# Kernel optimization log

Hardware: AMD Instinct MI355X
Metric: run time of the kernel (lower is better)

Reference implementation:

```python
import jax, jax.numpy as jnp
import numpy as np

ALPHA, BETA, GAMMA = 0.05, 0.95, 0.95   # list_weight
TANH_ALPHA = 2.0
GDEP = 2


def _gcn_rnn(x, adp, preA, W, b):
    # GCN type 'RNN': adaptive batched adj + predefined adj
    h = x
    outs = [h]
    for _ in range(GDEP):
        h = (ALPHA * x
             + BETA * jnp.einsum('nvc,nvw->nwc', h, adp)
             + GAMMA * jnp.einsum('nvc,vw->nwc', h, preA))
        outs.append(h)
    return jnp.concatenate(outs, -1) @ W + b


def _gcn_hyper(x, A, W, b):
    h = x
    outs = [h]
    for _ in range(GDEP):
        h = ALPHA * x + GAMMA * jnp.einsum('nvc,vw->nwc', h, A)
        outs.append(h)
    return jnp.concatenate(outs, -1) @ W + b


def _gcn_tgn(x, Ab, W, b):
    h = x
    outs = [h]
    for _ in range(GDEP):
        h = ALPHA * x + GAMMA * jnp.einsum('nvc,nvw->nwc', h, Ab)
        outs.append(h)
    return jnp.concatenate(outs, -1) @ W + b


def setup_inputs() -> dict:
    key = jax.random.key(0)
    ks = jax.random.split(key, 28)
    B, T, N, F = 16, 24, 512, 2
    H, E = 64, 16          # hidden_size, node embedding dim (dims_hyper[-1])
    TGN_OUT = 32
    D_ATTN = 4 * F         # TAttn default dim_out = 4 * dim_in
    p = lambda i, shape: jax.random.normal(ks[i], shape, dtype=jnp.float32) * 0.1
    return {
        'sample': jax.random.normal(ks[0], (B, T, N, F), dtype=jnp.float32),
        'predefined_A': jax.random.uniform(ks[1], (N, N), dtype=jnp.float32),
        'w_query': p(2, (F, D_ATTN)), 'w_key': p(3, (F, D_ATTN)),
        'attn_bias': p(4, (D_ATTN,)), 'attn_trans': p(5, (D_ATTN, 1)),
        'W_tgn': p(6, ((GDEP + 1) * F, TGN_OUT)), 'b_tgn': p(7, (TGN_OUT,)),
        'W_agg1': p(8, ((GDEP + 1) * H, E)), 'b_agg1': p(9, (E,)),
        'W_agg2': p(10, ((GDEP + 1) * H, E)), 'b_agg2': p(11, (E,)),
        'W_srcemb': p(12, (F, E)), 'b_srcemb': p(13, (E,)),
        'W_tgtemb': p(14, (F, E)), 'b_tgtemb': p(15, (E,)),
        'W_gz': p(16, ((GDEP + 1) * (F + H), H)), 'b_gz': p(17, (H,)),
        'W_gr': p(18, ((GDEP + 1) * (F + H), H)), 'b_gr': p(19, (H,)),
        'W_gc': p(20, ((GDEP + 1) * (F + H), H)), 'b_gc': p(21, (H,)),
        'W_short': p(22, (TGN_OUT, F)), 'b_short': p(23, (F,)),
        'W_long': p(24, (H, F)), 'b_long': p(25, (F,)),
        'W_mix': p(26, (TGN_OUT + H, F)), 'b_mix': p(27, (F,)),
    }


def reference(sample, predefined_A, w_query, w_key, attn_bias, attn_trans,
              W_tgn, b_tgn, W_agg1, b_agg1, W_agg2, b_agg2,
              W_srcemb, b_srcemb, W_tgtemb, b_tgtemb,
              W_gz, b_gz, W_gr, b_gr, W_gc, b_gc,
              W_short, b_short, W_long, b_long, W_mix, b_mix):
    B, T, N, F = sample.shape
    H = W_long.shape[0]
    A = predefined_A
    eye = jnp.eye(N, dtype=sample.dtype)

    def gru_step(hidden, graph):
        # hidden: [B,N,H], graph: [B,N,F]
        gs = _gcn_hyper(hidden, A, W_agg1, b_agg1)
        gt = _gcn_hyper(hidden, A, W_agg2, b_agg2)
        nv_s = jnp.tanh(TANH_ALPHA * (graph @ W_srcemb + b_srcemb) * gs)
        nv_t = jnp.tanh(TANH_ALPHA * (graph @ W_tgtemb + b_tgtemb) * gt)
        a = (jnp.einsum('bnd,bmd->bnm', nv_s, nv_t)
             - jnp.einsum('bnd,bmd->bnm', nv_t, nv_s))
        adp = jax.nn.relu(jnp.tanh(TANH_ALPHA * a)) + eye
        adp = adp / adp.sum(-1, keepdims=True)           # row-normalized [B,N,N]
        combined = jnp.concatenate([graph, hidden], -1)
        z = jax.nn.sigmoid(_gcn_rnn(combined, adp, A, W_gz, b_gz))
        r = jax.nn.sigmoid(_gcn_rnn(combined, adp, A, W_gr, b_gr))
        c = jnp.tanh(_gcn_rnn(jnp.concatenate([graph, r * hidden], -1), adp, A, W_gc, b_gc))
        return z * hidden + (1.0 - z) * c

    hidden = jnp.zeros((B, N, H), dtype=sample.dtype)
    graphs = jnp.moveaxis(sample[:, 0:T - 4:4], 1, 0)    # [T', B, N, F]
    hidden = jax.lax.scan(lambda h, g: (gru_step(h, g), None), hidden, graphs)[0]

    # temporal additive attention over the last 4 graphs (TAttn)
    src = sample[:, -4:]                                  # [B,4,N,F]
    tar = sample[:, -1]                                   # [B,N,F]
    q = (tar @ w_query)[:, None, :, None, :]              # [B,1,N,1,D]
    k = (src @ w_key)[:, :, None, :, :]                   # [B,4,1,N,D]
    scores = (jnp.tanh(q + k + attn_bias) @ attn_trans)[..., 0]   # [B,4,N,N]
    attn = jax.nn.softmax(scores, axis=-1)

    # single TGN layer: graph conv with (predefined + attention) adjacency
    Ab = A[None] + attn.reshape(-1, N, N)                 # [B*4,N,N]
    out = _gcn_tgn(src.reshape(-1, N, F), Ab, W_tgn, b_tgn)
    out = jax.nn.relu(out.reshape(B, 4, N, -1))
    tar = out.sum(axis=1)                                 # [B,N,TGN_OUT]

    gat_result = tar @ W_short + b_short                  # [B,N,F]
    hidden = gru_step(hidden, gat_result)
    gru_result = hidden @ W_long + b_long
    final_result = jnp.concatenate([tar, hidden], -1) @ W_mix + b_mix
    return gat_result, gru_result, final_result, attn
```

## Files before the change

### kernel.cpp

```cpp
#include <hip/hip_runtime.h>

#define ALPHA_C 0.05f
#define BETA_C  0.95f
#define GAMMA_C 0.95f

constexpr int B = 16, T = 24, N = 512, F = 2, H = 64, E = 16;
constexpr int DA = 8;
constexpr int CC = F + H;
constexpr int TGN_OC = 32;
constexpr int NPART = 4;
constexpr unsigned MEGA_LDS = 50176;
constexpr int NVB = 512;

__device__ __forceinline__ float fast_rcp(float x) { return __builtin_amdgcn_rcpf(x); }
__device__ __forceinline__ float fast_tanh(float x) {
    return 1.0f - 2.0f * fast_rcp(__expf(2.0f * x) + 1.0f);
}
__device__ __forceinline__ float fast_sigmoid(float x) {
    return fast_rcp(1.0f + __expf(-x));
}

__device__ __forceinline__ void gload16(const float* g, float* l)
{
    __builtin_amdgcn_global_load_lds((const __attribute__((address_space(1))) void*)g,
                                     (__attribute__((address_space(3))) void*)l, 16, 0, 0);
}

__device__ __forceinline__ void gridbar(unsigned* bar, unsigned nb)
{
    __syncthreads();
    if (threadIdx.x == 0) {
        __threadfence();
        unsigned g = __hip_atomic_load(&bar[1], __ATOMIC_RELAXED, __HIP_MEMORY_SCOPE_AGENT);
        unsigned arrived = __hip_atomic_fetch_add(&bar[0], 1u, __ATOMIC_ACQ_REL,
                                                  __HIP_MEMORY_SCOPE_AGENT);
        if (arrived == nb - 1u) {
            __hip_atomic_store(&bar[0], 0u, __ATOMIC_RELAXED, __HIP_MEMORY_SCOPE_AGENT);
            __hip_atomic_fetch_add(&bar[1], 1u, __ATOMIC_RELEASE, __HIP_MEMORY_SCOPE_AGENT);
        } else {
            while (__hip_atomic_load(&bar[1], __ATOMIC_ACQUIRE,
                                     __HIP_MEMORY_SCOPE_AGENT) == g)
                __builtin_amdgcn_s_sleep(4);
        }
        __threadfence();
    }
    __syncthreads();
}

__global__ void scaleA_kernel(const float* __restrict__ A, float* __restrict__ K1)
{
    int i = blockIdx.x * 256 + threadIdx.x;
    K1[i] = GAMMA_C * A[i];
}

__global__ __launch_bounds__(256) void k2_kernel(const float* __restrict__ A,
                                                 float* __restrict__ K2)
{
    __shared__ float rows[16][258];
    __shared__ float cols[256][17];
    const int tid = threadIdx.x;
    const int r0 = blockIdx.y * 16, c0 = blockIdx.x * 16;
    const int rr = tid >> 4, cc = tid & 15;
    float acc = 0.f;
    for (int k0 = 0; k0 < N; k0 += 256) {
#pragma unroll
        for (int it = 0; it < 4; ++it) {
            int l = it * 256 + tid;
            int row = l >> 6, k4 = (l & 63) << 2;
            *(float4*)&rows[row][k4] = *(const float4*)(A + (size_t)(r0 + row) * N + k0 + k4);
        }
#pragma unroll
        for (int it = 0; it < 4; ++it) {
            int l = it * 256 + tid;
            int k = l >> 2, c4 = (l & 3) << 2;
            *(float4*)&cols[k][c4] = *(const float4*)(A + (size_t)(k0 + k) * N + c0 + c4);
        }
        __syncthreads();
#pragma unroll 8
        for (int k = 0; k < 256; ++k) acc += rows[rr][k] * cols[k][cc];
        __syncthreads();
    }
    size_t i = (size_t)(r0 + rr) * N + c0 + cc;
    K2[i] = GAMMA_C * ALPHA_C * A[i] + GAMMA_C * GAMMA_C * acc;
}

template<bool INSUM>
__global__ __launch_bounds__(512) void bmm4_kernel(
    float* __restrict__ out, const float* __restrict__ x, const float* __restrict__ in,
    const float* __restrict__ M)
{
    __shared__ float sh_m[128][64];
    __shared__ float sh_h[64][68];
    constexpr int Crow = CC;
    const size_t pstr = (size_t)B * N * Crow;
    const int tid = threadIdx.x;
    const int b = blockIdx.z, w0 = blockIdx.x * 64, vq = blockIdx.y;
    const int cg = tid & 15;
    const int wg = tid >> 4;
    const int wid = tid >> 6;
    const int lane = tid & 63;

    float acc[2][4] = {{0,0,0,0},{0,0,0,0}};
    float ag[2] = {0.f, 0.f};

    const float* Mb = M + (size_t)b * N * N + (size_t)(vq * 128) * N + w0;
    const float* inb = in + (size_t)b * N * Crow;

#pragma unroll
    for (int it = 0; it < 4; ++it) {
        int row = it * 32 + wid * 4 + (lane >> 4);
        gload16(Mb + (size_t)row * N + ((lane & 15) << 2),
                &sh_m[0][0] + (it * 2048 + wid * 256));
    }

    for (int vt = 0; vt < 2; ++vt) {
        const int v0 = vq * 128 + vt * 64;
        {
            const float2* h0 = (const float2*)(inb + (size_t)v0 * Crow);
            for (int l = tid; l < 64 * 33; l += 512) {
                int row = l / 33, k = (l - row * 33) * 2;
                float2 v = h0[l];
                if (INSUM) {
#pragma unroll
                    for (int j = 1; j < NPART; ++j) {
                        float2 w = ((const float2*)(inb + (size_t)j * pstr + (size_t)v0 * Crow))[l];
                        v.x += w.x; v.y += w.y;
                    }
                }
                *(float2*)&sh_h[row][k] = v;
            }
        }
        __syncthreads();
#pragma unroll 8
        for (int j = 0; j < 64; ++j) {
            float2 mv = *(const float2*)&sh_m[vt * 64 + j][wg << 1];
            float4 hv = *(const float4*)&sh_h[j][cg << 2];
            acc[0][0] += mv.x * hv.x; acc[0][1] += mv.x * hv.y;
            acc[0][2] += mv.x * hv.z; acc[0][3] += mv.x * hv.w;
            acc[1][0] += mv.y * hv.x; acc[1][1] += mv.y * hv.y;
            acc[1][2] += mv.y * hv.z; acc[1][3] += mv.y * hv.w;
            if (cg < 2) {
                float gv = sh_h[j][64 + cg];
                ag[0] += mv.x * gv; ag[1] += mv.y * gv;
            }
        }
        if (vt == 0) __syncthreads();
    }
    float* outp = out + (size_t)vq * pstr + (size_t)b * N * Crow;
    const float* xb = x + (size_t)b * N * Crow;
#pragma unroll
    for (int r = 0; r < 2; ++r) {
        const int w = w0 + (wg << 1) + r;
        const size_t base = (size_t)w * Crow + (cg << 2);
        float o0 = acc[r][0], o1 = acc[r][1], o2 = acc[r][2], o3 = acc[r][3];
        if (vq == 0) {
            o0 += ALPHA_C * xb[base];     o1 += ALPHA_C * xb[base + 1];
            o2 += ALPHA_C * xb[base + 2]; o3 += ALPHA_C * xb[base + 3];
        }
        float2 lo = {o0, o1}, hi = {o2, o3};
        *(float2*)(outp + base) = lo;
        *(float2*)(outp + base + 2) = hi;
        if (cg < 2) {
            size_t gb = (size_t)w * Crow + 64 + cg;
            float v = ag[r];
            if (vq == 0) v += ALPHA_C * xb[gb];
            outp[gb] = v;
        }
    }
}

__global__ __launch_bounds__(512) void hyper5_kernel(
    float* __restrict__ P1, float* __restrict__ P2, const float* __restrict__ hidden,
    const float* __restrict__ K1, const float* __restrict__ K2)
{
    __shared__ float sh_m1[64][64];
    __shared__ float sh_m2[64][64];
    __shared__ float sh_h[64][64];
    const size_t pstr = (size_t)B * N * H;
    const int tid = threadIdx.x;
    const int b = blockIdx.z, w0 = blockIdx.x * 64, vq = blockIdx.y;
    const int cg = tid & 15;
    const int wg = tid >> 4;
    const int wid = tid >> 6;
    const int lane = tid & 63;

    float a1[2][4] = {{0,0,0,0},{0,0,0,0}};
    float a2[2][4] = {{0,0,0,0},{0,0,0,0}};
    const float* inb = hidden + (size_t)b * N * H;

    for (int vt = 0; vt < 2; ++vt) {
        const int v0 = vq * 128 + vt * 64;
#pragma unroll
        for (int it = 0; it < 2; ++it) {
            int row = it * 32 + wid * 4 + (lane >> 4);
            int c4 = (lane & 15) << 2;
// ... 177 lines not shown
    const float2* c2 = (const float2*)(base + nn0 * CC);
    const float2* p1b = (const float2*)(P1 + nn0 * CC);
    const float2* p2b = (const float2*)(P2 + nn0 * CC);
    for (int l = tid; l < 16 * 33; l += nthr) {
        int row = l & 15, kp = l >> 4;
        int idx = row * 33 + kp;
        float2 v = c2[idx];
        Xt[2 * kp][row] = v.x; Xt[2 * kp + 1][row] = v.y;
        float2 a = p1b[idx];
#pragma unroll
        for (int j = 1; j < NPART; ++j) {
            float2 w = ((const float2*)(P1 + (size_t)j * psC + nn0 * CC))[idx];
            a.x += w.x; a.y += w.y;
        }
        Xt[66 + 2 * kp][row] = a.x; Xt[66 + 2 * kp + 1][row] = a.y;
        float2 c = p2b[idx];
#pragma unroll
        for (int j = 1; j < NPART; ++j) {
            float2 w = ((const float2*)(P2 + (size_t)j * psC + nn0 * CC))[idx];
            c.x += w.x; c.y += w.y;
        }
        Xt[132 + 2 * kp][row] = c.x; Xt[132 + 2 * kp + 1][row] = c.y;
    }
}

__global__ __launch_bounds__(256) void zr5_kernel(
    const float* __restrict__ comb, const float* __restrict__ P1, const float* __restrict__ P2,
    const float* __restrict__ Wgz, const float* __restrict__ bgz,
    const float* __restrict__ Wgr, const float* __restrict__ bgr,
    const float* __restrict__ hidden,
    float* __restrict__ z, float* __restrict__ comb2)
{
    __shared__ float Xt[198][20];
    __shared__ float Wl[66][128];
    const int tid = threadIdx.x;
    const size_t nn0 = (size_t)blockIdx.x * 16;

    stage_xt(Xt, comb, P1, P2, nn0, tid, 256);

    const int cp = tid & 63;
    const int rg = tid >> 6;
    float2 bias = (cp < 32) ? *(const float2*)&bgz[2 * cp]
                            : *(const float2*)&bgr[2 * cp - 64];
    float acc[4][2];
#pragma unroll
    for (int r = 0; r < 4; ++r) { acc[r][0] = bias.x; acc[r][1] = bias.y; }

    for (int ch = 0; ch < 3; ++ch) {
        const int sk0 = ch * 66;
        for (int l = tid; l < 66 * 32; l += 256) {
            int j = l >> 5, q = l & 31;
            float4 w = (q < 16)
                ? ((const float4*)(Wgz + (size_t)(sk0 + j) * H))[q]
                : ((const float4*)(Wgr + (size_t)(sk0 + j) * H))[q - 16];
            *(float4*)&Wl[j][q << 2] = w;
        }
        __syncthreads();
#pragma unroll 6
        for (int j = 0; j < 66; ++j) {
            float4 xv = *(const float4*)&Xt[sk0 + j][rg << 2];
            float2 wv = *(const float2*)&Wl[j][cp << 1];
            acc[0][0] += xv.x * wv.x; acc[0][1] += xv.x * wv.y;
            acc[1][0] += xv.y * wv.x; acc[1][1] += xv.y * wv.y;
            acc[2][0] += xv.z * wv.x; acc[2][1] += xv.z * wv.y;
            acc[3][0] += xv.w * wv.x; acc[3][1] += xv.w * wv.y;
        }
        __syncthreads();
    }

    if (cp < 32) {
        const int oc = 2 * cp;
#pragma unroll
        for (int r = 0; r < 4; ++r) {
            size_t nn = nn0 + (rg << 2) + r;
            z[nn * H + oc]     = fast_sigmoid(acc[r][0]);
            z[nn * H + oc + 1] = fast_sigmoid(acc[r][1]);
        }
    } else {
        const int oc = 2 * cp - 64;
#pragma unroll
        for (int r = 0; r < 4; ++r) {
            size_t nn = nn0 + (rg << 2) + r;
            float h0 = hidden[nn * H + oc], h1 = hidden[nn * H + oc + 1];
            comb2[nn * CC + F + oc]     = fast_sigmoid(acc[r][0]) * h0;
            comb2[nn * CC + F + oc + 1] = fast_sigmoid(acc[r][1]) * h1;
        }
    }
    if (tid < 32) {
        int row = tid >> 1, f = tid & 1;
        comb2[(nn0 + row) * CC + f] = Xt[f][row];
    }
}

__global__ __launch_bounds__(256) void cup5_kernel(
    const float* __restrict__ comb2, const float* __restrict__ P1, const float* __restrict__ P2,
    const float* __restrict__ Wgc, const float* __restrict__ bgc,
    const float* __restrict__ z, float* __restrict__ hidden)
{
    __shared__ float Xt[198][20];
    __shared__ float Wl[66][64];
    const int tid = threadIdx.x;
    const size_t nn0 = (size_t)blockIdx.x * 16;

    stage_xt(Xt, comb2, P1, P2, nn0, tid, 256);

    const int cp = tid & 31;
    const int rg = tid >> 5;
    float2 bias = *(const float2*)&bgc[2 * cp];
    float acc[2][2];
#pragma unroll
    for (int r = 0; r < 2; ++r) { acc[r][0] = bias.x; acc[r][1] = bias.y; }

    for (int ch = 0; ch < 3; ++ch) {
        const int sk0 = ch * 66;
        for (int l = tid; l < 66 * 16; l += 256) {
            int j = l >> 4, q = l & 15;
            float4 w = ((const float4*)(Wgc + (size_t)(sk0 + j) * H))[q];
            *(float4*)&Wl[j][q << 2] = w;
        }
        __syncthreads();
#pragma unroll 6
        for (int j = 0; j < 66; ++j) {
            float2 xv = *(const float2*)&Xt[sk0 + j][rg << 1];
            float2 wv = *(const float2*)&Wl[j][cp << 1];
            acc[0][0] += xv.x * wv.x; acc[0][1] += xv.x * wv.y;
            acc[1][0] += xv.y * wv.x; acc[1][1] += xv.y * wv.y;
        }
        __syncthreads();
    }

    const int oc = 2 * cp;
#pragma unroll
    for (int r = 0; r < 2; ++r) {
        size_t nn = nn0 + (rg << 1) + r;
        float cv0 = fast_tanh(acc[r][0]);
        float cv1 = fast_tanh(acc[r][1]);
        float zv0 = z[nn * H + oc],     ho0 = hidden[nn * H + oc];
        float zv1 = z[nn * H + oc + 1], ho1 = hidden[nn * H + oc + 1];
        hidden[nn * H + oc]     = zv0 * ho0 + (1.0f - zv0) * cv0;
        hidden[nn * H + oc + 1] = zv1 * ho1 + (1.0f - zv1) * cv1;
    }
}

struct MegaArgs {
    const float* graph; long gstride; long gadv; int nsteps;
    const float *A;
    const float *Wa1, *ba1, *Wa2, *ba2, *Wsrc, *bsrc, *Wtgt, *btgt;
    const float *Wgz, *bgz, *Wgr, *bgr, *Wgc, *bgc;
    const float *K1, *K2;
    float *hidden, *nvs, *nvt, *Mcomb, *comb, *comb2, *z, *P1, *P2;
    unsigned* bar;
};

__device__ void ph_hyper(const MegaArgs& a, char* smem, int vb)
{
    float* sm1 = (float*)smem;
    float* sm2 = sm1 + 4096;
    float* shh = sm2 + 4096;
    const size_t pstr = (size_t)B * N * H;
    const int tid = threadIdx.x;
    const int w0 = (vb & 7) * 64, vq = (vb >> 3) & 3, b = vb >> 5;
    const int cg = tid & 15, wg = tid >> 4, wid = tid >> 6, lane = tid & 63;
    float a1[2][4] = {{0,0,0,0},{0,0,0,0}};
    float a2[2][4] = {{0,0,0,0},{0,0,0,0}};
    const float* inb = a.hidden + (size_t)b * N * H;

    for (int vt = 0; vt < 2; ++vt) {
        const int v0 = vq * 128 + vt * 64;
#pragma unroll
        for (int it = 0; it < 2; ++it) {
            int row = it * 32 + wid * 4 + (lane >> 4);
            int c4 = (lane & 15) << 2;
            int loff = it * 2048 + wid * 256;
            gload16(a.K1 + (size_t)(v0 + row) * N + w0 + c4, sm1 + loff);
            gload16(a.K2 + (size_t)(v0 + row) * N + w0 + c4, sm2 + loff);
            gload16(inb + (size_t)(v0 + row) * H + c4,       shh + loff);
        }
        __syncthreads();
#pragma unroll 8
        for (int j = 0; j < 64; ++j) {
            float2 m1 = *(const float2*)&sm1[j * 64 + (wg << 1)];
            float2 m2 = *(const float2*)&sm2[j * 64 + (wg << 1)];
            float4 hv = *(const float4*)&shh[j * 64 + (cg << 2)];
            a1[0][0] += m1.x * hv.x; a1[0][1] += m1.x * hv.y;
            a1[0][2] += m1.x * hv.z; a1[0][3] += m1.x * hv.w;
            a1[1][0] += m1.y * hv.x; a1[1][1] += m1.y * hv.y;
            a1[1][2] += m1.y * hv.z; a1[1][3] += m1.y * hv.w;
            a2[0][0] += m2.x * hv.x; a2[0][1] += m2.x * hv.y;
            a2[0][2] += m2.x * hv.z; a2[0][3] += m2.x * hv.w;
            a2[1][0] += m2.y * hv.x; a2[1][1] += m2.y * hv.y;
            a2[1][2] += m2.y * hv.z; a2[1][3] += m2.y * hv.w;
        }
        __syncthreads();
    }
    float* o1 = a.P1 + (size_t)vq * pstr + (size_t)b * N * H;
    float* o2 = a.P2 + (size_t)vq * pstr + (size_t)b * N * H;
#pragma unroll
    for (int r = 0; r < 2; ++r) {
        const int w = w0 + (wg << 1) + r;
        const size_t base = (size_t)w * H + (cg << 2);
        float4 v1 = {a1[r][0], a1[r][1], a1[r][2], a1[r][3]};
        float4 v2 = {a2[r][0], a2[r][1], a2[r][2], a2[r][3]};
        if (vq == 0) {
            float4 xv = *(const float4*)(inb + base);
            v1.x += ALPHA_C * xv.x; v1.y += ALPHA_C * xv.y;
            v1.z += ALPHA_C * xv.z; v1.w += ALPHA_C * xv.w;
            v2.x += ALPHA_C * xv.x; v2.y += ALPHA_C * xv.y;
            v2.z += ALPHA_C * xv.z; v2.w += ALPHA_C * xv.w;
        }
        *(float4*)(o1 + base) = v1;
        *(float4*)(o2 + base) = v2;
    }
}

__device__ void ph_gsgt(const MegaArgs& a, char* smem, const float* graph, int vb)
{
    constexpr size_t psH = (size_t)B * N * H;
    float (*sh)[196]  = (float(*)[196])smem;
    float (*W1t)[196] = (float(*)[196])(smem + 16 * 196 * 4);
    float (*W2t)[196] = (float(*)[196])(smem + 32 * 196 * 4);
    const int tid = threadIdx.x;
    const size_t nn0 = (size_t)vb * 16;
    for (int l = tid; l < 768; l += 512) {
        int seg = l >> 8, rr = (l >> 4) & 15, ee = l & 15;
        int f4 = ((int)nn0 + rr) * 16 + ee;
        float4 v;
        if (seg == 0) {
            v = ((const float4*)a.hidden)[f4];
        } else {
            const float* Pp = (seg == 1) ? a.P1 : a.P2;
            v = ((const float4*)Pp)[f4];
#pragma unroll
            for (int j = 1; j < NPART; ++j) {
                float4 w = ((const float4*)(Pp + (size_t)j * psH))[f4];
                v.x += w.x; v.y += w.y; v.z += w.z; v.w += w.w;
            }
        }
        *(float4*)&sh[rr][seg * 64 + (ee << 2)] = v;
    }
    for (int l = tid; l < 768; l += 512) {
        int sk = l >> 2, q = l & 3;
        float4 w1 = ((const float4*)a.Wa1)[l];
        float4 w2 = ((const float4*)a.Wa2)[l];
        W1t[4 * q + 0][sk] = w1.x; W1t[4 * q + 1][sk] = w1.y;
        W1t[4 * q + 2][sk] = w1.z; W1t[4 * q + 3][sk] = w1.w;
        W2t[4 * q + 0][sk] = w2.x; W2t[4 * q + 1][sk] = w2.y;
        W2t[4 * q + 2][sk] = w2.z; W2t[4 * q + 3][sk] = w2.w;
    }
    __syncthreads();
    const int e = tid & 15, row = (tid >> 4) & 15, which = tid >> 8;
    float acc = which ? a.ba2[e] : a.ba1[e];
    const float (*Wt_)[196] = which ? W2t : W1t;
#pragma unroll 8
    for (int sk = 0; sk < 192; sk += 4) {
        float4 xv = *(const float4*)&sh[row][sk];
        float4 wv = *(const float4*)&Wt_[e][sk];
        acc += xv.x * wv.x + xv.y * wv.y + xv.z * wv.z + xv.w * wv.w;
    }
    size_t nn = nn0 + row;
    int b = (int)(nn >> 9), n = (int)(nn & (N - 1));
    const float* gp = graph + (size_t)b * a.gstride + (size_t)n * F;
    float g0 = gp[0], g1 = gp[1];
    if (which == 0) {
        float es = g0 * a.Wsrc[e] + g1 * a.Wsrc[E + e] + a.bsrc[e];
        a.nvs[nn * E + e] = fast_tanh(2.0f * es * acc);
    } else {
        float et = g0 * a.Wtgt[e] + g1 * a.Wtgt[E + e] + a.btgt[e];
        a.nvt[nn * E + e] = fast_tanh(2.0f * et * acc);
    }
}

__device__ void ph_adp(const MegaArgs& a, char* smem, const float* graph, int vb)
{
    float (*red)[4] = (float(*)[4])smem;
    float* tot = (float*)(smem + 128);
    const int m = threadIdx.x;
    const int b = vb >> 5;
    const int ng = vb & 31;
    const float4* sm = (const float4*)(a.nvs + ((size_t)b * N + m) * E);
    const float4* tm = (const float4*)(a.nvt + ((size_t)b * N + m) * E);
    float4 smv[4], tmv[4];
#pragma unroll
    for (int dd = 0; dd < 4; ++dd) { smv[dd] = sm[dd]; tmv[dd] = tm[dd]; }

    for (int c = 0; c < 4; ++c) {
        const int n0 = (ng + 32 * c) * 4;
        const float4* sn = (const float4*)(a.nvs + ((size_t)b * N + n0) * E);
        const float4* tn = (const float4*)(a.nvt + ((size_t)b * N + n0) * E);
        float a1[4] = {0.f,0.f,0.f,0.f}, a2[4] = {0.f,0.f,0.f,0.f};
#pragma unroll
        for (int dd = 0; dd < 4; ++dd) {
#pragma unroll
            for (int r = 0; r < 4; ++r) {
                float4 snv = sn[r * 4 + dd], tnv = tn[r * 4 + dd];
                a1[r] += snv.x * tmv[dd].x + snv.y * tmv[dd].y + snv.z * tmv[dd].z + snv.w * tmv[dd].w;
                a2[r] += tnv.x * smv[dd].x + tnv.y * smv[dd].y + tnv.z * smv[dd].z + tnv.w * smv[dd].w;
            }
        }
        float p[4];
#pragma unroll
        for (int r = 0; r < 4; ++r) {
            float pv = fmaxf(fast_tanh(2.0f * (a1[r] - a2[r])), 0.0f);
            if (m == n0 + r) pv += 1.0f;
            p[r] = pv;
        }
        float sr[4] = {p[0], p[1], p[2], p[3]};
        for (int o = 32; o > 0; o >>= 1) {
#pragma unroll
            for (int r = 0; r < 4; ++r) sr[r] += __shfl_down(sr[r], o);
        }
        int wid = m >> 6, lane = m & 63;
        if (lane == 0) {
#pragma unroll
            for (int r = 0; r < 4; ++r) red[wid][r] = sr[r];
        }
        __syncthreads();
        if (m < 4) {
            float t = 0.f;
            for (int i = 0; i < 8; ++i) t += red[i][m];
            tot[m] = BETA_C * fast_rcp(t);
        }
        __syncthreads();
#pragma unroll
        for (int r = 0; r < 4; ++r)
            a.Mcomb[((size_t)b * N + n0 + r) * N + m] =
                GAMMA_C * a.A[(size_t)(n0 + r) * N + m] + p[r] * tot[r];
        if (m < 4 * CC) {
            int r = m / CC, k = m - r * CC;
            size_t nn = (size_t)b * N + n0 + r;
            float v;
            if (k < F) v = graph[(size_t)b * a.gstride + (size_t)(n0 + r) * F + k];
            else       v = a.hidden[nn * H + (k - F)];
            a.comb[nn * CC + k] = v;
        }
        __syncthreads();
    }
}

template<bool INSUM>
__device__ void ph_bmm(const MegaArgs& a, char* smem,
                       float* out, const float* x, const float* in, int vb)
{
    float* sh_m = (float*)smem;
    float (*sh_h)[68] = (float(*)[68])(smem + 128 * 64 * 4);
    constexpr int Crow = CC;
    const size_t pstr = (size_t)B * N * Crow;
    const int tid = threadIdx.x;
    const int w0 = (vb & 7) * 64, vq = (vb >> 3) & 3, b = vb >> 5;
    const int cg = tid & 15, wg = tid >> 4, wid = tid >> 6, lane = tid & 63;

    float acc[2][4] = {{0,0,0,0},{0,0,0,0}};
    float ag[2] = {0.f, 0.f};

    const float* Mb = a.Mcomb + (size_t)b * N * N + (size_t)(vq * 128) * N + w0;
    const float* inb = in + (size_t)b * N * Crow;

#pragma unroll
    for (int it = 0; it < 4; ++it) {
        int row = it * 32 + wid * 4 + (lane >> 4);
        gload16(Mb + (size_t)row * N + ((lane & 15) << 2),
                sh_m + (it * 2048 + wid * 256));
    }

    for (int vt = 0; vt < 2; ++vt) {
        const int v0 = vq * 128 + vt * 64;
        {
            const float2* h0 = (const float2*)(inb + (size_t)v0 * Crow);
            for (int l = tid; l < 64 * 33; l += 512) {
                int row = l / 33, k = (l - row * 33) * 2;
                float2 v = h0[l];
                if (INSUM) {
#pragma unroll
                    for (int j = 1; j < NPART; ++j) {
                        float2 w = ((const float2*)(inb + (size_t)j * pstr + (size_t)v0 * Crow))[l];
                        v.x += w.x; v.y += w.y;
                    }
                }
                *(float2*)&sh_h[row][k] = v;
            }
        }
        __syncthreads();
#pragma unroll 8
        for (int j = 0; j < 64; ++j) {
            float2 mv = *(const float2*)&sh_m[(vt * 64 + j) * 64 + (wg << 1)];
            float4 hv = *(const float4*)&sh_h[j][cg << 2];
            acc[0][0] += mv.x * hv.x; acc[0][1] += mv.x * hv.y;
            acc[0][2] += mv.x * hv.z; acc[0][3] += mv.x * hv.w;
            acc[1][0] += mv.y * hv.x; acc[1][1] += mv.y * hv.y;
            acc[1][2] += mv.y * hv.z; acc[1][3] += mv.y * hv.w;
            if (cg < 2) {
                float gv = sh_h[j][64 + cg];
                ag[0] += mv.x * gv; ag[1] += mv.y * gv;
            }
        }
        if (vt == 0) __syncthreads();
    }
    float* outp = out + (size_t)vq * pstr + (size_t)b * N * Crow;
    const float* xb = x + (size_t)b * N * Crow;
#pragma unroll
    for (int r = 0; r < 2; ++r) {
        const int w = w0 + (wg << 1) + r;
        const size_t base = (size_t)w * Crow + (cg << 2);
        float o0 = acc[r][0], o1 = acc[r][1], o2 = acc[r][2], o3 = acc[r][3];
        if (vq == 0) {
            o0 += ALPHA_C * xb[base];     o1 += ALPHA_C * xb[base + 1];
            o2 += ALPHA_C * xb[base + 2]; o3 += ALPHA_C * xb[base + 3];
        }
        float2 lo = {o0, o1}, hi = {o2, o3};
        *(float2*)(outp + base) = lo;
        *(float2*)(outp + base + 2) = hi;
        if (cg < 2) {
            size_t gb = (size_t)w * Crow + 64 + cg;
            float v = ag[r];
            if (vq == 0) v += ALPHA_C * xb[gb];
            outp[gb] = v;
        }
    }
}

__device__ void ph_zr(const MegaArgs& a, char* smem, int vb)
{
    float (*Xt)[20] = (float(*)[20])smem;
    float (*Wl)[128] = (float(*)[128])(smem + 198 * 20 * 4);
    const int tid = threadIdx.x;
    const size_t nn0 = (size_t)vb * 16;

    stage_xt(Xt, a.comb, a.P1, a.P2, nn0, tid, 512);

    const int cp = tid & 63;
    const int rg = tid >> 6;
    float2 bias = (cp < 32) ? *(const float2*)&a.bgz[2 * cp]
                            : *(const float2*)&a.bgr[2 * cp - 64];
    float acc[2][2] = {{bias.x, bias.y}, {bias.x, bias.y}};

    for (int ch = 0; ch < 3; ++ch) {
        const int sk0 = ch * 66;
        for (int l = tid; l < 66 * 32; l += 512) {
            int j = l >> 5, q = l & 31;
            float4 w = (q < 16)
                ? ((const float4*)(a.Wgz + (size_t)(sk0 + j) * H))[q]
                : ((const float4*)(a.Wgr + (size_t)(sk0 + j) * H))[q - 16];
            *(float4*)&Wl[j][q << 2] = w;
        }
        __syncthreads();
#pragma unroll 6
        for (int j = 0; j < 66; ++j) {
            float2 xv = *(const float2*)&Xt[sk0 + j][rg << 1];
            float2 wv = *(const float2*)&Wl[j][cp << 1];
            acc[0][0] += xv.x * wv.x; acc[0][1] += xv.x * wv.y;
            acc[1][0] += xv.y * wv.x; acc[1][1] += xv.y * wv.y;
        }
        __syncthreads();
    }

    if (cp < 32) {
        const int oc = 2 * cp;
#pragma unroll
        for (int r = 0; r < 2; ++r) {
            size_t nn = nn0 + (rg << 1) + r;
            a.z[nn * H + oc]     = fast_sigmoid(acc[r][0]);
            a.z[nn * H + oc + 1] = fast_sigmoid(acc[r][1]);
        }
    } else {
        const int oc = 2 * cp - 64;
#pragma unroll
        for (int r = 0; r < 2; ++r) {
            size_t nn = nn0 + (rg << 1) + r;
            float h0 = a.hidden[nn * H + oc], h1 = a.hidden[nn * H + oc + 1];
            a.comb2[nn * CC + F + oc]     = fast_sigmoid(acc[r][0]) * h0;
            a.comb2[nn * CC + F + oc + 1] = fast_sigmoid(acc[r][1]) * h1;
        }
    }
    if (tid < 32) {
        int row = tid >> 1, f = tid & 1;
        a.comb2[(nn0 + row) * CC + f] = Xt[f][row];
    }
}

__device__ void ph_cup(const MegaArgs& a, char* smem, int vb)
{
    float (*Xt)[20] = (float(*)[20])smem;
    float (*Wl)[64] = (float(*)[64])(smem + 198 * 20 * 4);
    const int tid = threadIdx.x;
    const size_t nn0 = (size_t)vb * 16;

    stage_xt(Xt, a.comb2, a.P1, a.P2, nn0, tid, 512);

    const int cp = tid & 31;
    const int rg = tid >> 5;
    float2 bias = *(const float2*)&a.bgc[2 * cp];
    float acc0 = bias.x, acc1 = bias.y;

    for (int ch = 0; ch < 3; ++ch) {
        const int sk0 = ch * 66;
        for (int l = tid; l < 66 * 16; l += 512) {
            int j = l >> 4, q = l & 15;
            float4 w = ((const float4*)(a.Wgc + (size_t)(sk0 + j) * H))[q];
            *(float4*)&Wl[j][q << 2] = w;
        }
        __syncthreads();
#pragma unroll 6
        for (int j = 0; j < 66; ++j) {
            float xv = Xt[sk0 + j][rg];
            float2 wv = *(const float2*)&Wl[j][cp << 1];
            acc0 += xv * wv.x; acc1 += xv * wv.y;
        }
        __syncthreads();
    }

    const int oc = 2 * cp;
    size_t nn = nn0 + rg;
    float cv0 = fast_tanh(acc0);
    float cv1 = fast_tanh(acc1);
    float zv0 = a.z[nn * H + oc],     ho0 = a.hidden[nn * H + oc];
    float zv1 = a.z[nn * H + oc + 1], ho1 = a.hidden[nn * H + oc + 1];
    a.hidden[nn * H + oc]     = zv0 * ho0 + (1.0f - zv0) * cv0;
    a.hidden[nn * H + oc + 1] = zv1 * ho1 + (1.0f - zv1) * cv1;
}

#define VB_LOOP(body) for (int vb = blockIdx.x; vb < NVB; vb += nbk) { body; __syncthreads(); }

__global__ __launch_bounds__(512, 2) void gru_mega(MegaArgs a)
{
    extern __shared__ float smem_f[];
    char* smem = (char*)smem_f;
    const int nbk = gridDim.x;
    unsigned* bar = a.bar;
    const float* graph = a.graph;
    for (int s = 0; s < a.nsteps; ++s) {
        VB_LOOP(ph_hyper(a, smem, vb));                              gridbar(bar, nbk);
        VB_LOOP(ph_gsgt(a, smem, graph, vb));                        gridbar(bar, nbk);
        VB_LOOP(ph_adp(a, smem, graph, vb));                         gridbar(bar, nbk);
        VB_LOOP(ph_bmm<false>(a, smem, a.P1, a.comb, a.comb, vb));   gridbar(bar, nbk);
        VB_LOOP(ph_bmm<true>(a, smem, a.P2, a.comb, a.P1, vb));      gridbar(bar, nbk);
        VB_LOOP(ph_zr(a, smem, vb));                                 gridbar(bar, nbk);
        VB_LOOP(ph_bmm<false>(a, smem, a.P1, a.comb2, a.comb2, vb)); gridbar(bar, nbk);
        VB_LOOP(ph_bmm<true>(a, smem, a.P2, a.comb2, a.P1, vb));     gridbar(bar, nbk);
        VB_LOOP(ph_cup(a, smem, vb));                                gridbar(bar, nbk);
        graph += a.gadv;
    }
}

__global__ void qk_kernel(const float* __restrict__ sample,
                          const float* __restrict__ wq, const float* __restrict__ wk,
                          const float* __restrict__ attn_bias,
                          float* __restrict__ q, float* __restrict__ kk)
{
    int idx = blockIdx.x * 256 + threadIdx.x;
    if (idx < B * N * DA) {
        int d = idx & 7;
        int n = (idx >> 3) & (N - 1);
        int b = idx >> 12;
        const float* tar = sample + (((size_t)b * T + (T - 1)) * N + n) * F;
        q[idx] = tar[0] * wq[d] + tar[1] * wq[DA + d] + attn_bias[d];
    } else {
        int j = idx - B * N * DA;
        int d = j & 7;
        int n = (j >> 3) & (N - 1);
        int t = (j >> 12) & 3;
        int b = j >> 14;
        const float* s = sample + (((size_t)b * T + (T - 4 + t)) * N + n) * F;
        kk[j] = s[0] * wk[d] + s[1] * wk[DA + d];
    }
}

__global__ __launch_bounds__(256) void scores3_kernel(
    const float* __restrict__ q, const float* __restrict__ kk,
    const float* __restrict__ trans, float* __restrict__ attn)
{
    int bt = blockIdx.y;
    int b = bt >> 2;
    int rbase = blockIdx.x * 16;
    int wid = threadIdx.x >> 6, lane = threadIdx.x & 63;
    const float* kkbt = kk + (size_t)bt * N * DA;
    float* attnbt = attn + (size_t)bt * N * N;
    float tr[8];
#pragma unroll
    for (int d = 0; d < 8; ++d) tr[d] = trans[d];
    for (int i = 0; i < 4; ++i) {
        int n = rbase + wid * 4 + i;
        const float* qp = q + ((size_t)b * N + n) * DA;
        float4 qa = *(const float4*)qp, qb = *(const float4*)(qp + 4);
        float ev[8]; float ssum = 0.f;
#pragma unroll
        for (int k = 0; k < 8; ++k) {
            const float* kp = kkbt + (size_t)(k * 64 + lane) * DA;
            float4 ka = *(const float4*)kp, kb = *(const float4*)(kp + 4);
            float s = fast_tanh(qa.x + ka.x) * tr[0] + fast_tanh(qa.y + ka.y) * tr[1]
                    + fast_tanh(qa.z + ka.z) * tr[2] + fast_tanh(qa.w + ka.w) * tr[3]
                    + fast_tanh(qb.x + kb.x) * tr[4] + fast_tanh(qb.y + kb.y) * tr[5]
                    + fast_tanh(qb.z + kb.z) * tr[6] + fast_tanh(qb.w + kb.w) * tr[7];
            ev[k] = __expf(s);
            ssum += ev[k];
        }
        for (int o = 32; o > 0; o >>= 1) ssum += __shfl_down(ssum, o);
        ssum = __shfl(ssum, 0);
        float rinv = fast_rcp(ssum);
#pragma unroll
        for (int k = 0; k < 8; ++k)
            attnbt[(size_t)n * N + k * 64 + lane] = ev[k] * rinv;
    }
}

__global__ __launch_bounds__(256) void tgn2_kernel(
    const float* __restrict__ A, const float* __restrict__ attn,
    const float* __restrict__ hbase, long hsB, long hsT,
    const float* __restrict__ xbase, long xsB, long xsT,
    float* __restrict__ out)
{
    __shared__ float sh_m[64][65];
    __shared__ float sh_h[64][2];
    int bt = blockIdx.y;
    int w0 = blockIdx.x * 64;
    int tid = threadIdx.x;
    int wl = tid >> 2, c = tid & 1, vh = (tid >> 1) & 1;
    const float* hp = hbase + (size_t)(bt >> 2) * hsB + (size_t)(bt & 3) * hsT;
    const float* ap = attn + (size_t)bt * N * N;
    float acc = 0.f;
    for (int vt = 0; vt < 8; ++vt) {
        int v0 = vt * 64;
#pragma unroll
        for (int it = 0; it < 16; ++it) {
            int l = it * 256 + tid;
            int vr = l >> 6, wc = l & 63;
            size_t gi = (size_t)(v0 + vr) * N + (w0 + wc);
            sh_m[wc][vr] = A[gi] + ap[gi];
        }
        if (tid < 128) sh_h[tid >> 1][tid & 1] = hp[(size_t)(v0 + (tid >> 1)) * F + (tid & 1)];
        __syncthreads();
#pragma unroll
        for (int jj = 0; jj < 32; ++jj) {
            int j = vh * 32 + jj;
            acc += sh_m[wl][j] * sh_h[j][c];
        }
        __syncthreads();
    }
    acc += __shfl_xor(acc, 2);
    if (vh == 0) {
        const float* xp = xbase + (size_t)(bt >> 2) * xsB + (size_t)(bt & 3) * xsT;
        out[((size_t)bt * N + w0 + wl) * F + c] =
            ALPHA_C * xp[(size_t)(w0 + wl) * F + c] + GAMMA_C * acc;
    }
}

__global__ __launch_bounds__(256) void tgn_out_gat_kernel(
    const float* __restrict__ sample,
    const float* __restrict__ th1, const float* __restrict__ th2,
    const float* __restrict__ Wt, const float* __restrict__ bt_,
    const float* __restrict__ Ws, const float* __restrict__ bs,
    float* __restrict__ tar32, float* __restrict__ out0)
{
    __shared__ float sh_t[8][33];
    const int tid = threadIdx.x;
    const int oc = tid & 31;
    const int r = tid >> 5;
    const size_t nn = (size_t)blockIdx.x * 8 + r;
    const int n = (int)(nn & (N - 1));
    const int b = (int)(nn >> 9);
    float acc = 0.f;
    for (int t = 0; t < 4; ++t) {
        int bt = b * 4 + t;
        const float* s = sample + (((size_t)b * T + (T - 4 + t)) * N + n) * F;
        size_t rr = ((size_t)bt * N + n) * F;
        float v = bt_[oc];
        v += s[0] * Wt[0 * TGN_OC + oc] + s[1] * Wt[1 * TGN_OC + oc];
        v += th1[rr] * Wt[2 * TGN_OC + oc] + th1[rr + 1] * Wt[3 * TGN_OC + oc];
        v += th2[rr] * Wt[4 * TGN_OC + oc] + th2[rr + 1] * Wt[5 * TGN_OC + oc];
        acc += fmaxf(v, 0.0f);
    }
    tar32[nn * TGN_OC + oc] = acc;
    sh_t[r][oc] = acc;
    __syncthreads();
    if (tid < 16) {
        int row = tid >> 1, f = tid & 1;
        size_t nn2 = (size_t)blockIdx.x * 8 + row;
        float g = bs[f];
#pragma unroll
        for (int k = 0; k < TGN_OC; ++k) g += sh_t[row][k] * Ws[(size_t)k * F + f];
        out0[nn2 * F + f] = g;
    }
}

__global__ void final_kernel(const float* __restrict__ hidden, const float* __restrict__ tar32,
                             const float* __restrict__ Wl, const float* __restrict__ bl,
                             const float* __restrict__ Wm, const float* __restrict__ bm,
                             float* __restrict__ dout_gru, float* __restrict__ dout_fin)
{
    int idx = blockIdx.x * 256 + threadIdx.x;
    int f = idx & 1;
    int nn = idx >> 1;
    const float* hp = hidden + (size_t)nn * H;
    const float* tp = tar32 + (size_t)nn * TGN_OC;
    float g = bl[f], fin = bm[f];
    for (int k = 0; k < H; ++k) g += hp[k] * Wl[(size_t)k * F + f];
    for (int k = 0; k < TGN_OC; ++k) fin += tp[k] * Wm[(size_t)k * F + f];
    for (int k = 0; k < H; ++k) fin += hp[k] * Wm[(size_t)(TGN_OC + k) * F + f];
    dout_gru[idx] = g;
    dout_fin[idx] = fin;
}

namespace {
struct Ptrs {
    const float *sample, *A, *wq, *wk, *attn_bias, *attn_trans, *Wt, *bt_;
    const float *Wa1, *ba1, *Wa2, *ba2, *Wsrc, *bsrc, *Wtgt, *btgt;
    const float *Wgz, *bgz, *Wgr, *bgr, *Wgc, *bgc, *Wsh, *bsh, *Wl, *bl, *Wm, *bm;
    float *hidden, *nvs, *nvt, *Mcomb, *K1, *K2, *comb, *comb2, *z, *P1, *P2;
    float *q, *kk, *th1, *th2, *tar32;
    unsigned* bar;
};

void gru_step(hipStream_t stream, const Ptrs& p, const float* graph, long gstride)
{
    dim3 bg(8, NPART, B);
    hyper5_kernel<<<bg, 512, 0, stream>>>(p.P1, p.P2, p.hidden, p.K1, p.K2);
    gsgt5_kernel<<<B * N / 16, 256, 0, stream>>>(
        p.hidden, p.P1, p.P2, p.Wa1, p.ba1, p.Wa2, p.ba2, graph, gstride,
        p.Wsrc, p.bsrc, p.Wtgt, p.btgt, p.nvs, p.nvt);
    adp3_kernel<<<dim3(N / 4, B), 512, 0, stream>>>(
        p.nvs, p.nvt, p.A, p.hidden, graph, gstride, p.Mcomb, p.comb);
    bmm4_kernel<false><<<bg, 512, 0, stream>>>(p.P1, p.comb, p.comb, p.Mcomb);
    bmm4_kernel<true><<<bg, 512, 0, stream>>>(p.P2, p.comb, p.P1, p.Mcomb);
    zr5_kernel<<<B * N / 16, 256, 0, stream>>>(
        p.comb, p.P1, p.P2, p.Wgz, p.bgz, p.Wgr, p.bgr, p.hidden, p.z, p.comb2);
    bmm4_kernel<false><<<bg, 512, 0, stream>>>(p.P1, p.comb2, p.comb2, p.Mcomb);
    bmm4_kernel<true><<<bg, 512, 0, stream>>>(p.P2, p.comb2, p.P1, p.Mcomb);
    cup5_kernel<<<B * N / 16, 256, 0, stream>>>(
        p.comb2, p.P1, p.P2, p.Wgc, p.bgc, p.z, p.hidden);
}
}

extern "C" void kernel_launch(void* const* d_in, const int* in_sizes, int n_in,
                              void* d_out, int out_size, void* d_ws, size_t ws_size,
                              hipStream_t stream)
{
    (void)in_sizes; (void)n_in; (void)out_size; (void)ws_size;
    Ptrs p;
    p.sample = (const float*)d_in[0];
    p.A      = (const float*)d_in[1];
    p.wq     = (const float*)d_in[2];
    p.wk     = (const float*)d_in[3];
    p.attn_bias  = (const float*)d_in[4];
    p.attn_trans = (const float*)d_in[5];
    p.Wt  = (const float*)d_in[6];
    p.bt_ = (const float*)d_in[7];
    p.Wa1 = (const float*)d_in[8];
    p.ba1 = (const float*)d_in[9];
    p.Wa2 = (const float*)d_in[10];
    p.ba2 = (const float*)d_in[11];
    p.Wsrc = (const float*)d_in[12];
    p.bsrc = (const float*)d_in[13];
    p.Wtgt = (const float*)d_in[14];
    p.btgt = (const float*)d_in[15];
    p.Wgz = (const float*)d_in[16];
    p.bgz = (const float*)d_in[17];
    p.Wgr = (const float*)d_in[18];
    p.bgr = (const float*)d_in[19];
    p.Wgc = (const float*)d_in[20];
    p.bgc = (const float*)d_in[21];
    p.Wsh = (const float*)d_in[22];
    p.bsh = (const float*)d_in[23];
    p.Wl  = (const float*)d_in[24];
    p.bl  = (const float*)d_in[25];
    p.Wm  = (const float*)d_in[26];
    p.bm  = (const float*)d_in[27];

    float* ws = (float*)d_ws;
    size_t off = 0;
    auto alloc = [&](size_t nelem) { float* r = ws + off; off += nelem; return r; };
    p.hidden = alloc((size_t)B * N * H);
    p.nvs    = alloc((size_t)B * N * E);
    p.nvt    = alloc((size_t)B * N * E);
    p.Mcomb  = alloc((size_t)B * N * N);
    p.K1     = alloc((size_t)N * N);
    p.K2     = alloc((size_t)N * N);
    p.comb   = alloc((size_t)B * N * CC);
    p.comb2  = alloc((size_t)B * N * CC);
    p.z      = alloc((size_t)B * N * H);
    p.P1     = alloc((size_t)NPART * B * N * CC);
    p.P2     = alloc((size_t)NPART * B * N * CC);
    p.q      = alloc((size_t)B * N * DA);
    p.kk     = alloc((size_t)B * 4 * N * DA);
    p.th1    = alloc((size_t)B * 4 * N * F);
    p.th2    = alloc((size_t)B * 4 * N * F);
    p.tar32  = alloc((size_t)B * N * TGN_OC);
    p.bar    = (unsigned*)alloc(16);

    float* out = (float*)d_out;
    float* out_gat = out;
    float* out_gru = out + (size_t)B * N * F;
    float* out_fin = out + (size_t)2 * B * N * F;
    float* out_attn = out + (size_t)3 * B * N * F;

    hipMemsetAsync(p.hidden, 0, (size_t)B * N * H * sizeof(float), stream);
    hipMemsetAsync(p.bar, 0, 16 * sizeof(float), stream);
    scaleA_kernel<<<N * N / 256, 256, 0, stream>>>(p.A, p.K1);
    k2_kernel<<<dim3(32, 32), 256, 0, stream>>>(p.A, p.K2);

    int mp = 0, nb = 0;
    hipDeviceGetAttribute(&mp, hipDeviceAttributeMultiprocessorCount, 0);
    hipOccupancyMaxActiveBlocksPerMultiprocessor(&nb, gru_mega, 512, (size_t)MEGA_LDS);
    int grid = nb * mp;
    if (grid > NVB) grid = NVB;
    bool mega_ok = (grid >= 64);

    MegaArgs ma;
    ma.graph = p.sample; ma.gstride = (long)T * N * F; ma.gadv = (long)4 * N * F;
    ma.nsteps = 5;
    ma.A = p.A;
    ma.Wa1 = p.Wa1; ma.ba1 = p.ba1; ma.Wa2 = p.Wa2; ma.ba2 = p.ba2;
    ma.Wsrc = p.Wsrc; ma.bsrc = p.bsrc; ma.Wtgt = p.Wtgt; ma.btgt = p.btgt;
    ma.Wgz = p.Wgz; ma.bgz = p.bgz; ma.Wgr = p.Wgr; ma.bgr = p.bgr;
    ma.Wgc = p.Wgc; ma.bgc = p.bgc;
    ma.K1 = p.K1; ma.K2 = p.K2;
    ma.hidden = p.hidden; ma.nvs = p.nvs; ma.nvt = p.nvt; ma.Mcomb = p.Mcomb;
    ma.comb = p.comb; ma.comb2 = p.comb2; ma.z = p.z; ma.P1 = p.P1; ma.P2 = p.P2;
    ma.bar = p.bar;

    if (mega_ok) {
        gru_mega<<<grid, 512, MEGA_LDS, stream>>>(ma);
    } else {
        for (int i = 0; i < 5; ++i)
            gru_step(stream, p, p.sample + (size_t)(4 * i) * N * F, (long)T * N * F);
    }

    qk_kernel<<<(B * N * DA + B * 4 * N * DA) / 256, 256, 0, stream>>>(
        p.sample, p.wq, p.wk, p.attn_bias, p.q, p.kk);
    scores3_kernel<<<dim3(32, 64), 256, 0, stream>>>(p.q, p.kk, p.attn_trans, out_attn);

    const float* srcbase = p.sample + (size_t)(T - 4) * N * F;
    tgn2_kernel<<<dim3(8, 64), 256, 0, stream>>>(
        p.A, out_attn, srcbase, (long)T * N * F, (long)N * F,
        srcbase, (long)T * N * F, (long)N * F, p.th1);
    tgn2_kernel<<<dim3(8, 64), 256, 0, stream>>>(
        p.A, out_attn, p.th1, (long)4 * N * F, (long)N * F,
        srcbase, (long)T * N * F, (long)N * F, p.th2);
    tgn_out_gat_kernel<<<B * N / 8, 256, 0, stream>>>(
        p.sample, p.th1, p.th2, p.Wt, p.bt_, p.Wsh, p.bsh, p.tar32, out_gat);

    MegaArgs ma2 = ma;
    ma2.graph = out_gat; ma2.gstride = (long)N * F; ma2.gadv = 0; ma2.nsteps = 1;
    if (mega_ok) {
        gru_mega<<<grid, 512, MEGA_LDS, stream>>>(ma2);
    } else {
        gru_step(stream, p, out_gat, (long)N * F);
    }

    final_kernel<<<(B * N * F) / 256, 256, 0, stream>>>(
        p.hidden, p.tar32, p.Wl, p.bl, p.Wm, p.bm, out_gru, out_fin);
}
```

Before: 1.270 ms.

## Replace grid-wide barriers with per-batch group barriers in persistent GRU kernel

The persistent GRU megakernel now launches exactly 512 blocks, one per (batch, tile) pair, and each batch's 32 blocks synchronise on their own barrier counter instead of a single grid-wide barrier. Every phase only depends on data from the same batch, so batches can progress independently and barrier contention on one atomic is spread over 16 counters. The spin sleep interval is also shortened. This requires all 512 blocks to be co-resident, otherwise the kernel deadlocks. The launch guard now checks for full residency and falls back to the multi-kernel path if it is not met.

```diff
diff --git a/kernel.cpp b/kernel.cpp
--- a/kernel.cpp
+++ b/kernel.cpp
@@ -26,7 +26,7 @@
                                      (__attribute__((address_space(3))) void*)l, 16, 0, 0);
 }
 
-__device__ __forceinline__ void gridbar(unsigned* bar, unsigned nb)
+__device__ __forceinline__ void groupbar(unsigned* bar)
 {
     __syncthreads();
     if (threadIdx.x == 0) {
@@ -34,13 +34,13 @@
         unsigned g = __hip_atomic_load(&bar[1], __ATOMIC_RELAXED, __HIP_MEMORY_SCOPE_AGENT);
         unsigned arrived = __hip_atomic_fetch_add(&bar[0], 1u, __ATOMIC_ACQ_REL,
                                                   __HIP_MEMORY_SCOPE_AGENT);
-        if (arrived == nb - 1u) {
+        if (arrived == 31u) {
             __hip_atomic_store(&bar[0], 0u, __ATOMIC_RELAXED, __HIP_MEMORY_SCOPE_AGENT);
             __hip_atomic_fetch_add(&bar[1], 1u, __ATOMIC_RELEASE, __HIP_MEMORY_SCOPE_AGENT);
         } else {
             while (__hip_atomic_load(&bar[1], __ATOMIC_ACQUIRE,
                                      __HIP_MEMORY_SCOPE_AGENT) == g)
-                __builtin_amdgcn_s_sleep(4);
+                __builtin_amdgcn_s_sleep(2);
         }
         __threadfence();
     }
@@ -524,14 +524,14 @@
     unsigned* bar;
 };
 
-__device__ void ph_hyper(const MegaArgs& a, char* smem, int vb)
+__device__ void ph_hyper(const MegaArgs& a, char* smem, int b, int vb)
 {
     float* sm1 = (float*)smem;
     float* sm2 = sm1 + 4096;
     float* shh = sm2 + 4096;
     const size_t pstr = (size_t)B * N * H;
     const int tid = threadIdx.x;
-    const int w0 = (vb & 7) * 64, vq = (vb >> 3) & 3, b = vb >> 5;
+    const int w0 = (vb & 7) * 64, vq = vb >> 3;
     const int cg = tid & 15, wg = tid >> 4, wid = tid >> 6, lane = tid & 63;
     float a1[2][4] = {{0,0,0,0},{0,0,0,0}};
     float a2[2][4] = {{0,0,0,0},{0,0,0,0}};
@@ -585,14 +585,14 @@
     }
 }
 
-__device__ void ph_gsgt(const MegaArgs& a, char* smem, const float* graph, int vb)
+__device__ void ph_gsgt(const MegaArgs& a, char* smem, const float* graph, int b, int vb)
 {
     constexpr size_t psH = (size_t)B * N * H;
     float (*sh)[196]  = (float(*)[196])smem;
     float (*W1t)[196] = (float(*)[196])(smem + 16 * 196 * 4);
     float (*W2t)[196] = (float(*)[196])(smem + 32 * 196 * 4);
     const int tid = threadIdx.x;
-    const size_t nn0 = (size_t)vb * 16;
+    const size_t nn0 = (size_t)b * N + (size_t)vb * 16;
     for (int l = tid; l < 768; l += 512) {
         int seg = l >> 8, rr = (l >> 4) & 15, ee = l & 15;
         int f4 = ((int)nn0 + rr) * 16 + ee;
@@ -630,7 +630,7 @@
         acc += xv.x * wv.x + xv.y * wv.y + xv.z * wv.z + xv.w * wv.w;
     }
     size_t nn = nn0 + row;
-    int b = (int)(nn >> 9), n = (int)(nn & (N - 1));
+    int n = (int)(nn & (N - 1));
     const float* gp = graph + (size_t)b * a.gstride + (size_t)n * F;
     float g0 = gp[0], g1 = gp[1];
     if (which == 0) {
@@ -642,13 +642,12 @@
     }
 }
 
-__device__ void ph_adp(const MegaArgs& a, char* smem, const float* graph, int vb)
+__device__ void ph_adp(const MegaArgs& a, char* smem, const float* graph, int b, int vb)
 {
     float (*red)[4] = (float(*)[4])smem;
     float* tot = (float*)(smem + 128);
     const int m = threadIdx.x;
-    const int b = vb >> 5;
-    const int ng = vb & 31;
+    const int ng = vb;
     const float4* sm = (const float4*)(a.nvs + ((size_t)b * N + m) * E);
     const float4* tm = (const float4*)(a.nvt + ((size_t)b * N + m) * E);
     float4 smv[4], tmv[4];
@@ -711,14 +710,14 @@
 
 template<bool INSUM>
 __device__ void ph_bmm(const MegaArgs& a, char* smem,
-                       float* out, const float* x, const float* in, int vb)
+                       float* out, const float* x, const float* in, int b, int vb)
 {
     float* sh_m = (float*)smem;
     float (*sh_h)[68] = (float(*)[68])(smem + 128 * 64 * 4);
     constexpr int Crow = CC;
     const size_t pstr = (size_t)B * N * Crow;
     const int tid = threadIdx.x;
-    const int w0 = (vb & 7) * 64, vq = (vb >> 3) & 3, b = vb >> 5;
+    const int w0 = (vb & 7) * 64, vq = vb >> 3;
     const int cg = tid & 15, wg = tid >> 4, wid = tid >> 6, lane = tid & 63;
 
     float acc[2][4] = {{0,0,0,0},{0,0,0,0}};
@@ -790,12 +789,12 @@
     }
 }
 
-__device__ void ph_zr(const MegaArgs& a, char* smem, int vb)
+__device__ void ph_zr(const MegaArgs& a, char* smem, int b, int vb)
 {
     float (*Xt)[20] = (float(*)[20])smem;
     float (*Wl)[128] = (float(*)[128])(smem + 198 * 20 * 4);
     const int tid = threadIdx.x;
-    const size_t nn0 = (size_t)vb * 16;
+    const size_t nn0 = (size_t)b * N + (size_t)vb * 16;
 
     stage_xt(Xt, a.comb, a.P1, a.P2, nn0, tid, 512);
 
@@ -849,12 +848,12 @@
     }
 }
 
-__device__ void ph_cup(const MegaArgs& a, char* smem, int vb)
+__device__ void ph_cup(const MegaArgs& a, char* smem, int b, int vb)
 {
     float (*Xt)[20] = (float(*)[20])smem;
     float (*Wl)[64] = (float(*)[64])(smem + 198 * 20 * 4);
     const int tid = threadIdx.x;
-    const size_t nn0 = (size_t)vb * 16;
+    const size_t nn0 = (size_t)b * N + (size_t)vb * 16;
 
     stage_xt(Xt, a.comb2, a.P1, a.P2, nn0, tid, 512);
 
@@ -890,25 +889,24 @@
     a.hidden[nn * H + oc + 1] = zv1 * ho1 + (1.0f - zv1) * cv1;
 }
 
-#define VB_LOOP(body) for (int vb = blockIdx.x; vb < NVB; vb += nbk) { body; __syncthreads(); }
-
 __global__ __launch_bounds__(512, 2) void gru_mega(MegaArgs a)
 {
     extern __shared__ float smem_f[];
     char* smem = (char*)smem_f;
-    const int nbk = gridDim.x;
-    unsigned* bar = a.bar;
+    const int b  = blockIdx.x >> 5;
+    const int vb = blockIdx.x & 31;
+    unsigned* bar = a.bar + (size_t)b * 32;
     const float* graph = a.graph;
     for (int s = 0; s < a.nsteps; ++s) {
-        VB_LOOP(ph_hyper(a, smem, vb));                              gridbar(bar, nbk);
-        VB_LOOP(ph_gsgt(a, smem, graph, vb));                        gridbar(bar, nbk);
-        VB_LOOP(ph_adp(a, smem, graph, vb));                         gridbar(bar, nbk);
-        VB_LOOP(ph_bmm<false>(a, smem, a.P1, a.comb, a.comb, vb));   gridbar(bar, nbk);
-        VB_LOOP(ph_bmm<true>(a, smem, a.P2, a.comb, a.P1, vb));      gridbar(bar, nbk);
-        VB_LOOP(ph_zr(a, smem, vb));                                 gridbar(bar, nbk);
-        VB_LOOP(ph_bmm<false>(a, smem, a.P1, a.comb2, a.comb2, vb)); gridbar(bar, nbk);
-        VB_LOOP(ph_bmm<true>(a, smem, a.P2, a.comb2, a.P1, vb));     gridbar(bar, nbk);
-        VB_LOOP(ph_cup(a, smem, vb));                                gridbar(bar, nbk);
+        ph_hyper(a, smem, b, vb);                               groupbar(bar);
+        ph_gsgt(a, smem, graph, b, vb);                         groupbar(bar);
+        ph_adp(a, smem, graph, b, vb);                          groupbar(bar);
+        ph_bmm<false>(a, smem, a.P1, a.comb, a.comb, b, vb);    groupbar(bar);
+        ph_bmm<true>(a, smem, a.P2, a.comb, a.P1, b, vb);       groupbar(bar);
+        ph_zr(a, smem, b, vb);                                  groupbar(bar);
+        ph_bmm<false>(a, smem, a.P1, a.comb2, a.comb2, b, vb);  groupbar(bar);
+        ph_bmm<true>(a, smem, a.P2, a.comb2, a.P1, b, vb);      groupbar(bar);
+        ph_cup(a, smem, b, vb);                                 groupbar(bar);
         graph += a.gadv;
     }
 }
@@ -1155,7 +1153,7 @@
     p.th1    = alloc((size_t)B * 4 * N * F);
     p.th2    = alloc((size_t)B * 4 * N * F);
     p.tar32  = alloc((size_t)B * N * TGN_OC);
-    p.bar    = (unsigned*)alloc(16);
+    p.bar    = (unsigned*)alloc(512);
 
     float* out = (float*)d_out;
     float* out_gat = out;
@@ -1164,16 +1162,14 @@
     float* out_attn = out + (size_t)3 * B * N * F;
 
     hipMemsetAsync(p.hidden, 0, (size_t)B * N * H * sizeof(float), stream);
-    hipMemsetAsync(p.bar, 0, 16 * sizeof(float), stream);
+    hipMemsetAsync(p.bar, 0, 512 * sizeof(unsigned), stream);
     scaleA_kernel<<<N * N / 256, 256, 0, stream>>>(p.A, p.K1);
     k2_kernel<<<dim3(32, 32), 256, 0, stream>>>(p.A, p.K2);
 
     int mp = 0, nb = 0;
     hipDeviceGetAttribute(&mp, hipDeviceAttributeMultiprocessorCount, 0);
     hipOccupancyMaxActiveBlocksPerMultiprocessor(&nb, gru_mega, 512, (size_t)MEGA_LDS);
-    int grid = nb * mp;
-    if (grid > NVB) grid = NVB;
-    bool mega_ok = (grid >= 64);
+    bool mega_ok = ((long)nb * mp >= NVB);
 
     MegaArgs ma;
     ma.graph = p.sample; ma.gstride = (long)T * N * F; ma.gadv = (long)4 * N * F;
@@ -1189,7 +1185,7 @@
     ma.bar = p.bar;
 
     if (mega_ok) {
-        gru_mega<<<grid, 512, MEGA_LDS, stream>>>(ma);
+        gru_mega<<<NVB, 512, MEGA_LDS, stream>>>(ma);
     } else {
         for (int i = 0; i < 5; ++i)
             gru_step(stream, p, p.sample + (size_t)(4 * i) * N * F, (long)T * N * F);
@@ -1212,7 +1208,7 @@
     MegaArgs ma2 = ma;
     ma2.graph = out_gat; ma2.gstride = (long)N * F; ma2.gadv = 0; ma2.nsteps = 1;
     if (mega_ok) {
-        gru_mega<<<grid, 512, MEGA_LDS, stream>>>(ma2);
+        gru_mega<<<NVB, 512, MEGA_LDS, stream>>>(ma2);
     } else {
         gru_step(stream, p, out_gat, (long)N * F);
     }
```

After: 1.268 ms. About the same (-0.1%).
